# Optimization experiments

Measured on AMD Instinct MI355X. Metric: run time of the kernel, lower is better.

The kernel has to match this reference:

```python
import jax, jax.numpy as jnp
import numpy as np

N = 50000      # nodes
E = 800000     # edges
D_IN = 128     # raw feature dim
H = 96         # hidden_channels
K = 8          # experts
L = 4          # num_layers
C = 40         # classes


def setup_inputs() -> dict:
    key = jax.random.key(0)
    ks = jax.random.split(key, 10)
    stdv = 1.0 / np.sqrt(H)
    inp = {
        'x': jax.random.normal(ks[0], (N, D_IN), dtype=jnp.float32),
        'edge_index': jax.random.randint(ks[1], (2, E), 0, N, dtype=jnp.int64),
        # fcs[0]: Linear(d, hidden); fcs[1]: Linear(hidden, c)
        'fc0_w': jax.random.normal(ks[2], (D_IN, H), dtype=jnp.float32) * 0.05,
        'fc0_b': jnp.zeros((H,), dtype=jnp.float32),
        'fc1_w': jax.random.normal(ks[3], (H, C), dtype=jnp.float32) * 0.05,
        'fc1_b': jnp.zeros((C,), dtype=jnp.float32),
        # context_enc (method='node'): per-layer Linear(hidden, K)
        'ctx_w': jax.random.normal(ks[4], (L, H, K), dtype=jnp.float32) * 0.05,
        'ctx_b': jnp.zeros((L, K), dtype=jnp.float32),
        # GraphMultiConvolution weights: [L, K, hidden, hidden], uniform(-stdv, stdv)
        'conv_w': jax.random.uniform(ks[5], (L, K, H, H), dtype=jnp.float32,
                                     minval=-stdv, maxval=stdv),
    }
    return inp


def reference(x, edge_index, fc0_w, fc0_b, fc1_w, fc1_b, ctx_w, ctx_b, conv_w):
    # eval-mode forward (training=False): no dropout, softmax routing
    row = edge_index[0]
    col = edge_index[1]
    h = jax.nn.relu(x @ fc0_w + fc0_b)                     # [N, H]
    for i in range(L):
        # routing logits and soft expert weights z: [N, K]
        z = jax.nn.softmax(h @ ctx_w[i] + ctx_b[i], axis=-1)
        # spmm aggregation: hi[r] = sum over edges (r, c) of h[c]
        hi = jax.ops.segment_sum(h[col], row, num_segments=N)  # [N, H]
        # K-expert batched matmul: [N, K, H]
        outs = jnp.einsum('nd,kdo->nko', hi, conv_w[i])
        # gumbel/softmax-weighted combine + residual
        out = jnp.einsum('nk,nko->no', z, outs) + h
        h = jax.nn.relu(out)
    return h @ fc1_w + fc1_b                               # [N, C]
```

## Files before the change

### kernel.cpp

```cpp
#include <hip/hip_runtime.h>

#define N_NODES 50000
#define N_EDGES 800000
#define DIN     128
#define H       96
#define K_EXP   8
#define L_LAYERS 4
#define C_OUT   40

#define GSZ 6250

typedef _Float16 f16;
typedef f16 f16x2 __attribute__((ext_vector_type(2)));
typedef f16 f16x4 __attribute__((ext_vector_type(4)));
typedef f16 f16x8 __attribute__((ext_vector_type(8)));
typedef float f32x4 __attribute__((ext_vector_type(4)));


__global__ __launch_bounds__(256) void count_p(const int* __restrict__ row,
                                               int* __restrict__ deg,
                                               int* __restrict__ p, int e) {
    int i = blockIdx.x * blockDim.x + threadIdx.x;
    if (i < e) p[i] = atomicAdd(&deg[row[i]], 1);
}

__global__ __launch_bounds__(1024) void scanA(const int* __restrict__ deg,
                                              int* __restrict__ rowptr,
                                              int* __restrict__ partial, int n) {
    __shared__ int wsum[16];
    int tid  = threadIdx.x;
    int lane = tid & 63, wid = tid >> 6;
    int idx = blockIdx.x * 1024 + tid;
    int v = (idx < n) ? deg[idx] : 0;
    int s = v;
    #pragma unroll
    for (int off = 1; off < 64; off <<= 1) {
        int t = __shfl_up(s, off, 64);
        if (lane >= off) s += t;
    }
    if (lane == 63) wsum[wid] = s;
    __syncthreads();
    if (wid == 0 && lane < 16) {
        int w = wsum[lane];
        #pragma unroll
        for (int off = 1; off < 16; off <<= 1) {
            int t = __shfl_up(w, off, 16);
            if (lane >= off) w += t;
        }
        wsum[lane] = w;
    }
    __syncthreads();
    int waveoff = (wid == 0) ? 0 : wsum[wid - 1];
    if (idx < n) rowptr[idx + 1] = waveoff + s;
    if (tid == 1023) partial[blockIdx.x] = waveoff + s;
}

__global__ __launch_bounds__(1024) void scanC(int* __restrict__ rowptr,
                                              const int* __restrict__ partial,
                                              int nb, int n) {
    __shared__ int boff_s;
    int tid = threadIdx.x;
    if (tid < 64) {
        int v = (tid < nb && tid < (int)blockIdx.x) ? partial[tid] : 0;
        #pragma unroll
        for (int off = 32; off >= 1; off >>= 1) v += __shfl_xor(v, off, 64);
        if (tid == 0) boff_s = v;
    }
    __syncthreads();
    int boff = boff_s;
    int idx = blockIdx.x * 1024 + tid;
    if (idx == 0) rowptr[0] = 0;
    if (idx < n) rowptr[idx + 1] += boff;
}

__global__ __launch_bounds__(256) void scatter_store_xcd(const int* __restrict__ row,
                                                         const int* __restrict__ col,
                                                         const int* __restrict__ p,
                                                         const int* __restrict__ rowptr,
                                                         int* __restrict__ csr, int e) {
    int g = blockIdx.x & 7;
    int rlo = g * GSZ, rhi = rlo + GSZ;
    int stride = (gridDim.x >> 3) * 256;
    for (int i = (blockIdx.x >> 3) * 256 + threadIdx.x; i < e; i += stride) {
        int r = row[i];
        if (r >= rlo && r < rhi)
            csr[rowptr[r] + p[i]] = col[i];
    }
}


#define CONV_TOT (L_LAYERS * K_EXP * H * H)
#define FC0_TOT  (DIN * H)
#define FC1_TOT  (48 * H)

__global__ void convert_all(const float* __restrict__ conv_w,
                            const float* __restrict__ fc0_w,
                            const float* __restrict__ fc1_w,
                            f16* __restrict__ wfrag, f16* __restrict__ fc0t,
                            f16* __restrict__ fc1t) {
    int i = blockIdx.x * blockDim.x + threadIdx.x;
    if (i < CONV_TOT) {
        int o = i % H;
        int t = i / H;
        int d = t % H;
        int lk = t / H;
        int ct = o >> 4, lc = o & 15;
        int ks = d >> 5, quad = (d >> 3) & 3, j = d & 7;
        wfrag[(size_t)lk * 9216 + ct * 1536 + ks * 512 + (quad * 16 + lc) * 8 + j] =
            (f16)conv_w[i];
    } else if (i < CONV_TOT + FC0_TOT) {
        int j = i - CONV_TOT;
        int o = j % H, d = j / H;
        fc0t[o * DIN + d] = (f16)fc0_w[j];
    } else if (i < CONV_TOT + FC0_TOT + FC1_TOT) {
        int j = i - CONV_TOT - FC0_TOT;
        int o = j / H, d = j % H;
        fc1t[j] = (o < C_OUT) ? (f16)fc1_w[d * C_OUT + o] : (f16)0.f;
    }
}


#define SPMM_BLOCKS ((N_NODES + 31) / 32)
#define CTX_BLOCKS  ((N_NODES + 255) / 256)

__global__ __launch_bounds__(256) void layer_pre(const f16* __restrict__ h16,
                                                 const int* __restrict__ rowptr,
                                                 const int* __restrict__ csr,
                                                 f16* __restrict__ hi16,
                                                 const float* __restrict__ cw,
                                                 const float* __restrict__ cb,
                                                 float* __restrict__ zt, int n) {
    __shared__ float ws[H * K_EXP];
    __shared__ float bs[K_EXP];
    int tid = threadIdx.x;
    if ((int)blockIdx.x < SPMM_BLOCKS) {
        int r0 = blockIdx.x * 32 + (tid >> 4);
        int r1 = r0 + 16;
        int li = tid & 15;
        if (r0 >= n) return;
        int j0 = rowptr[r0], e0 = rowptr[r0 + 1];
        int j1 = 0, e1 = 0;
        if (r1 < n) { j1 = rowptr[r1]; e1 = rowptr[r1 + 1]; }
        bool act = li < 12;
        float accA[8] = {}, accB[8] = {};
        for (;;) {
            int m0 = e0 - j0; if (m0 > 16) m0 = 16;
            int m1 = e1 - j1; if (m1 > 16) m1 = 16;
            if (m0 <= 0 && m1 <= 0) break;
            int c0 = 0, c1 = 0;
            if (li < m0) c0 = csr[j0 + li];
            if (li < m1) c1 = csr[j1 + li];
            int mm = m0 > m1 ? m0 : m1;
            int t = 0;
            for (; t + 2 <= mm; t += 2) {
                int cc0a = __shfl(c0, t, 16),     cc1a = __shfl(c1, t, 16);
                int cc0b = __shfl(c0, t + 1, 16), cc1b = __shfl(c1, t + 1, 16);
                bool a0a = act && (t < m0),     a1a = act && (t < m1);
                bool a0b = act && (t + 1 < m0), a1b = act && (t + 1 < m1);
                f16x8 v0a = {}, v1a = {}, v0b = {}, v1b = {};
                if (a0a) v0a = *(const f16x8*)(h16 + (size_t)cc0a * H + li * 8);
                if (a1a) v1a = *(const f16x8*)(h16 + (size_t)cc1a * H + li * 8);
                if (a0b) v0b = *(const f16x8*)(h16 + (size_t)cc0b * H + li * 8);
                if (a1b) v1b = *(const f16x8*)(h16 + (size_t)cc1b * H + li * 8);
                if (a0a) {
                    #pragma unroll
                    for (int q = 0; q < 8; q++) accA[q] += (float)v0a[q];
                }
                if (a1a) {
                    #pragma unroll
                    for (int q = 0; q < 8; q++) accB[q] += (float)v1a[q];
                }
                if (a0b) {
                    #pragma unroll
                    for (int q = 0; q < 8; q++) accA[q] += (float)v0b[q];
                }
                if (a1b) {
                    #pragma unroll
                    for (int q = 0; q < 8; q++) accB[q] += (float)v1b[q];
                }
            }
            if (t < mm) {
                int cc0 = __shfl(c0, t, 16), cc1 = __shfl(c1, t, 16);
                bool a0 = act && (t < m0), a1 = act && (t < m1);
                f16x8 v0 = {}, v1 = {};
                if (a0) v0 = *(const f16x8*)(h16 + (size_t)cc0 * H + li * 8);
                if (a1) v1 = *(const f16x8*)(h16 + (size_t)cc1 * H + li * 8);
                if (a0) {
                    #pragma unroll
                    for (int q = 0; q < 8; q++) accA[q] += (float)v0[q];
                }
                if (a1) {
                    #pragma unroll
                    for (int q = 0; q < 8; q++) accB[q] += (float)v1[q];
                }
            }
            j0 += m0; j1 += m1;
        }
        if (act) {
            f16x8 oA;
            #pragma unroll
            for (int q = 0; q < 8; q++) oA[q] = (f16)accA[q];
            *(f16x8*)(hi16 + (size_t)r0 * H + li * 8) = oA;
            if (r1 < n) {
                f16x8 oB;
                #pragma unroll
                for (int q = 0; q < 8; q++) oB[q] = (f16)accB[q];
                *(f16x8*)(hi16 + (size_t)r1 * H + li * 8) = oB;
            }
        }
    } else {
        for (int t = tid; t < H * K_EXP; t += 256) ws[t] = cw[t];
        if (tid < K_EXP) bs[tid] = cb[tid];
        __syncthreads();
        int node = ((int)blockIdx.x - SPMM_BLOCKS) * 256 + tid;
        if (node >= n) return;
        float acc[K_EXP];
        #pragma unroll
        for (int k = 0; k < K_EXP; k++) acc[k] = bs[k];
        const f16* hr = h16 + (size_t)node * H;
        #pragma unroll 3
        for (int c8 = 0; c8 < 12; c8++) {
            f16x8 v = *(const f16x8*)(hr + c8 * 8);
            #pragma unroll
            for (int j = 0; j < 8; j++) {
                float hv = (float)v[j];
                int d = c8 * 8 + j;
                #pragma unroll
                for (int k = 0; k < K_EXP; k++) acc[k] += hv * ws[d * K_EXP + k];
            }
        }
        float mx = acc[0];
        #pragma unroll
        for (int k = 1; k < K_EXP; k++) mx = fmaxf(mx, acc[k]);
        float s = 0.f;
        #pragma unroll
        for (int k = 0; k < K_EXP; k++) { acc[k] = __expf(acc[k] - mx); s += acc[k]; }
        float inv = 1.f / s;
        #pragma unroll
        for (int k = 0; k < K_EXP; k++)
            zt[(size_t)k * N_NODES + node] = acc[k] * inv;
    }
}


#define FPAD 136

__global__ __launch_bounds__(256) void fc0_kernel(const float* __restrict__ x,
                                                  const f16* __restrict__ fc0t,
                                                  const float* __restrict__ b,
                                                  f16* __restrict__ h16, int n) {
    __shared__ f16 As[64 * FPAD];
    __shared__ f16 Ws[96 * FPAD];
    int tid = threadIdx.x;
    int l = tid & 63, w = tid >> 6;
    int quad = l >> 4, lc = l & 15;
    int row0 = blockIdx.x * 64;

    for (int t = tid; t < 2048; t += 256) {
        int m = t >> 5, c4 = (t & 31) * 4;
        int gr = row0 + m;
        float4 v = {0.f, 0.f, 0.f, 0.f};
        if (gr < n) v = *(const float4*)(x + (size_t)gr * DIN + c4);
        f16x4 h4 = {(f16)v.x, (f16)v.y, (f16)v.z, (f16)v.w};
        *(f16x4*)&As[m * FPAD + c4] = h4;
    }
    for (int t = tid; t < 1536; t += 256) {
        int o = t >> 4, c8 = (t & 15) * 8;
        *(f16x8*)&Ws[o * FPAD + c8] = *(const f16x8*)(fc0t + o * DIN + c8);
    }
    __syncthreads();

    f16x8 afr[4];
    #pragma unroll
    for (int ks = 0; ks < 4; ks++)
        afr[ks] = *(const f16x8*)&As[(16 * w + lc) * FPAD + ks * 32 + quad * 8];

    f32x4 acc[6] = {};
    #pragma unroll
    for (int ct = 0; ct < 6; ct++) {
        #pragma unroll
        for (int ks = 0; ks < 4; ks++) {
            f16x8 bfr = *(const f16x8*)&Ws[(ct * 16 + lc) * FPAD + ks * 32 + quad * 8];
            acc[ct] = __builtin_amdgcn_mfma_f32_16x16x32_f16(afr[ks], bfr, acc[ct], 0, 0, 0);
        }
    }

    int m0 = 16 * w + quad * 4;
    #pragma unroll
    for (int r = 0; r < 4; r++) {
        int gr = row0 + m0 + r;
        if (gr < n) {
            #pragma unroll
            for (int ct = 0; ct < 6; ct++) {
                int o = ct * 16 + lc;
                h16[(size_t)gr * H + o] = (f16)fmaxf(acc[ct][r] + b[o], 0.f);
            }
        }
    }
}


#define EG_STAGE 2
#define EG_HALFS (EG_STAGE * 9216)

__global__ __launch_bounds__(256) void expert_gemm(const f16* __restrict__ hi16,
                                                   const f16* __restrict__ hin16,
                                                   const f16* __restrict__ wfrag,
                                                   const float* __restrict__ zt,
                                                   f16* __restrict__ hout16, int n) {
    __shared__ f16 Wl[EG_HALFS];
    int tid = threadIdx.x;
    int l = tid & 63, w = tid >> 6;
    int quad = l >> 4, lc = l & 15;
    int wrow0 = blockIdx.x * 64 + w * 16;

    f16x8 afr[3];
    #pragma unroll
    for (int ks = 0; ks < 3; ks++)
        afr[ks] = *(const f16x8*)(hi16 + (size_t)(wrow0 + lc) * H + ks * 32 + quad * 8);

    f32x4 acc[6] = {};

    for (int kb = 0; kb < K_EXP; kb += EG_STAGE) {
        __syncthreads();
        const f16* src = wfrag + (size_t)kb * 9216;
        for (int t = tid; t < EG_HALFS / 8; t += 256)
            *(f16x8*)&Wl[t * 8] = *(const f16x8*)(src + t * 8);
        __syncthreads();

        #pragma unroll
        for (int k2 = 0; k2 < EG_STAGE; k2++) {
            int k = kb + k2;
            f32x4 zf = *(const f32x4*)(zt + (size_t)k * N_NODES + wrow0 + quad * 4);
            #pragma unroll
            for (int ct = 0; ct < 6; ct++) {
                f16x8 b0 = *(const f16x8*)&Wl[k2 * 9216 + ct * 1536 + 0 * 512 + l * 8];
                f16x8 b1 = *(const f16x8*)&Wl[k2 * 9216 + ct * 1536 + 1 * 512 + l * 8];
                f16x8 b2 = *(const f16x8*)&Wl[k2 * 9216 + ct * 1536 + 2 * 512 + l * 8];
                f32x4 tmp = {};
                tmp = __builtin_amdgcn_mfma_f32_16x16x32_f16(afr[0], b0, tmp, 0, 0, 0);
                tmp = __builtin_amdgcn_mfma_f32_16x16x32_f16(afr[1], b1, tmp, 0, 0, 0);
                tmp = __builtin_amdgcn_mfma_f32_16x16x32_f16(afr[2], b2, tmp, 0, 0, 0);
                acc[ct] += zf * tmp;
            }
        }
    }

    #pragma unroll
    for (int r = 0; r < 4; r++) {
        int gr = wrow0 + quad * 4 + r;
        if (gr < n) {
            #pragma unroll
            for (int ct = 0; ct < 6; ct++) {
                int o = ct * 16 + lc;
                float v = fmaxf(acc[ct][r] + (float)hin16[(size_t)gr * H + o], 0.f);
                hout16[(size_t)gr * H + o] = (f16)v;
            }
        }
    }
}


#define APAD 104

__global__ __launch_bounds__(256) void fc1_kernel(const f16* __restrict__ h16,
                                                  const f16* __restrict__ fc1t,
                                                  const float* __restrict__ b,
                                                  float* __restrict__ out, int n) {
    __shared__ f16 As[64 * APAD];
    __shared__ f16 Ws[48 * APAD];
    int tid = threadIdx.x;
    int l = tid & 63, w = tid >> 6;
    int quad = l >> 4, lc = l & 15;
    int row0 = blockIdx.x * 64;

    for (int t = tid; t < 768; t += 256) {
        int m = t / 12, c8 = (t % 12) * 8;
        int gr = row0 + m;
        f16x8 v = {};
        if (gr < n) v = *(const f16x8*)(h16 + (size_t)gr * H + c8);
        *(f16x8*)&As[m * APAD + c8] = v;
    }
    for (int t = tid; t < 576; t += 256) {
        int o = t / 12, c8 = (t % 12) * 8;
        *(f16x8*)&Ws[o * APAD + c8] = *(const f16x8*)(fc1t + o * H + c8);
    }
    __syncthreads();

    f16x8 afr[3];
    #pragma unroll
    for (int ks = 0; ks < 3; ks++)
        afr[ks] = *(const f16x8*)&As[(16 * w + lc) * APAD + ks * 32 + quad * 8];

    f32x4 acc[3] = {};
    #pragma unroll
    for (int ct = 0; ct < 3; ct++) {
        #pragma unroll
        for (int ks = 0; ks < 3; ks++) {
            f16x8 bfr = *(const f16x8*)&Ws[(ct * 16 + lc) * APAD + ks * 32 + quad * 8];
            acc[ct] = __builtin_amdgcn_mfma_f32_16x16x32_f16(afr[ks], bfr, acc[ct], 0, 0, 0);
        }
    }

    int m0 = 16 * w + quad * 4;
    #pragma unroll
    for (int r = 0; r < 4; r++) {
        int gr = row0 + m0 + r;
        if (gr < n) {
            #pragma unroll
            for (int ct = 0; ct < 3; ct++) {
                int o = ct * 16 + lc;
                if (o < C_OUT)
                    out[(size_t)gr * C_OUT + o] = acc[ct][r] + b[o];
            }
        }
    }
}


extern "C" void kernel_launch(void* const* d_in, const int* in_sizes, int n_in,
                              void* d_out, int out_size, void* d_ws, size_t ws_size,
                              hipStream_t stream) {
    const float* x      = (const float*)d_in[0];
    const int*   ei     = (const int*)d_in[1];
    const float* fc0_w  = (const float*)d_in[2];
    const float* fc0_b  = (const float*)d_in[3];
    const float* fc1_w  = (const float*)d_in[4];
    const float* fc1_b  = (const float*)d_in[5];
    const float* ctx_w  = (const float*)d_in[6];
    const float* ctx_b  = (const float*)d_in[7];
    const float* conv_w = (const float*)d_in[8];
    float* out = (float*)d_out;

    const size_t NH = (size_t)N_NODES * H;

    float* zbuf = (float*)d_ws;
    f16*   h16a = (f16*)(zbuf + (size_t)N_NODES * K_EXP);
    f16*   h16b = h16a + NH;
    f16*   hi16 = h16b + NH;
    f16*   wfrag= hi16 + NH;
    f16*   fc0t = wfrag + CONV_TOT;
    f16*   fc1t = fc0t + FC0_TOT;
    int* rowptr = (int*)(fc1t + FC1_TOT);
    int* deg    = rowptr + (N_NODES + 1);
    int* csr    = deg + N_NODES;
    int* prank  = csr + N_EDGES;
    int* partial  = prank + N_EDGES;

    const int* row = ei;
    const int* col = ei + N_EDGES;

    hipMemsetAsync(deg, 0, sizeof(int) * N_NODES, stream);

    count_p<<<(N_EDGES + 255) / 256, 256, 0, stream>>>(row, deg, prank, N_EDGES);
    int nsb = (N_NODES + 1023) / 1024;
    scanA<<<nsb, 1024, 0, stream>>>(deg, rowptr, partial, N_NODES);
    scanC<<<nsb, 1024, 0, stream>>>(rowptr, partial, nsb, N_NODES);
    scatter_store_xcd<<<1024, 256, 0, stream>>>(row, col, prank, rowptr, csr, N_EDGES);

    int ctotal = CONV_TOT + FC0_TOT + FC1_TOT;
    convert_all<<<(ctotal + 255) / 256, 256, 0, stream>>>(conv_w, fc0_w, fc1_w, wfrag, fc0t, fc1t);

    int gemm_grid = (N_NODES + 63) / 64;
    fc0_kernel<<<gemm_grid, 256, 0, stream>>>(x, fc0t, fc0_b, h16a, N_NODES);

    f16* hcur = h16a;
    f16* hnext = h16b;
    for (int i = 0; i < L_LAYERS; i++) {
        layer_pre<<<SPMM_BLOCKS + CTX_BLOCKS, 256, 0, stream>>>(
            hcur, rowptr, csr, hi16,
            ctx_w + (size_t)i * H * K_EXP, ctx_b + (size_t)i * K_EXP, zbuf, N_NODES);
        expert_gemm<<<gemm_grid, 256, 0, stream>>>(
            hi16, hcur, wfrag + (size_t)i * K_EXP * H * H, zbuf, hnext, N_NODES);
        f16* t = hcur; hcur = hnext; hnext = t;
    }
    fc1_kernel<<<gemm_grid, 256, 0, stream>>>(hcur, fc1t, fc1_b, out, N_NODES);
}
```

Measured before the change: 375.7 us.

## Bucket CSR neighbors by source-column range and sync blocks per bucket in SpMM

Builds the CSR with each row's edges split into 7 buckets keyed by the source column's high bits (8192-node ranges), so every row is stored as per-bucket segments. The SpMM walks the buckets in order and puts a block barrier after each one, so all warps in a block gather from the same slice of h at the same time, aiming for better cache locality. The cost is a scan over 8x more segment counters (400k entries with a larger partial-sum reduction), extra rowptr loads and barriers per row in SpMM, and more loop overhead for the short per-bucket edge lists.

```diff
diff --git a/kernel.cpp b/kernel.cpp
--- a/kernel.cpp
+++ b/kernel.cpp
@@ -10,6 +10,11 @@
 
 #define GSZ 6250
 
+#define NB_SHIFT 13
+#define NBUCK    7
+#define SEG_STRIDE 8
+#define NSEG (N_NODES * SEG_STRIDE)
+
 typedef _Float16 f16;
 typedef f16 f16x2 __attribute__((ext_vector_type(2)));
 typedef f16 f16x4 __attribute__((ext_vector_type(4)));
@@ -18,10 +23,14 @@
 
 
 __global__ __launch_bounds__(256) void count_p(const int* __restrict__ row,
+                                               const int* __restrict__ col,
                                                int* __restrict__ deg,
                                                int* __restrict__ p, int e) {
     int i = blockIdx.x * blockDim.x + threadIdx.x;
-    if (i < e) p[i] = atomicAdd(&deg[row[i]], 1);
+    if (i < e) {
+        int seg = row[i] * SEG_STRIDE + (col[i] >> NB_SHIFT);
+        p[i] = atomicAdd(&deg[seg], 1);
+    }
 }
 
 __global__ __launch_bounds__(1024) void scanA(const int* __restrict__ deg,
@@ -61,7 +70,8 @@
     __shared__ int boff_s;
     int tid = threadIdx.x;
     if (tid < 64) {
-        int v = (tid < nb && tid < (int)blockIdx.x) ? partial[tid] : 0;
+        int v = 0;
+        for (int j = tid; j < (int)blockIdx.x; j += 64) v += partial[j];
         #pragma unroll
         for (int off = 32; off >= 1; off >>= 1) v += __shfl_xor(v, off, 64);
         if (tid == 0) boff_s = v;
@@ -83,8 +93,11 @@
     int stride = (gridDim.x >> 3) * 256;
     for (int i = (blockIdx.x >> 3) * 256 + threadIdx.x; i < e; i += stride) {
         int r = row[i];
-        if (r >= rlo && r < rhi)
-            csr[rowptr[r] + p[i]] = col[i];
+        if (r >= rlo && r < rhi) {
+            int c = col[i];
+            int seg = r * SEG_STRIDE + (c >> NB_SHIFT);
+            csr[rowptr[seg] + p[i]] = c;
+        }
     }
 }
 
@@ -137,71 +150,75 @@
         int r0 = blockIdx.x * 32 + (tid >> 4);
         int r1 = r0 + 16;
         int li = tid & 15;
-        if (r0 >= n) return;
-        int j0 = rowptr[r0], e0 = rowptr[r0 + 1];
-        int j1 = 0, e1 = 0;
-        if (r1 < n) { j1 = rowptr[r1]; e1 = rowptr[r1 + 1]; }
+        bool v0 = r0 < n, v1 = r1 < n;
+        int base0 = r0 * SEG_STRIDE, base1 = r1 * SEG_STRIDE;
         bool act = li < 12;
         float accA[8] = {}, accB[8] = {};
-        for (;;) {
-            int m0 = e0 - j0; if (m0 > 16) m0 = 16;
-            int m1 = e1 - j1; if (m1 > 16) m1 = 16;
-            if (m0 <= 0 && m1 <= 0) break;
-            int c0 = 0, c1 = 0;
-            if (li < m0) c0 = csr[j0 + li];
-            if (li < m1) c1 = csr[j1 + li];
-            int mm = m0 > m1 ? m0 : m1;
-            int t = 0;
-            for (; t + 2 <= mm; t += 2) {
-                int cc0a = __shfl(c0, t, 16),     cc1a = __shfl(c1, t, 16);
-                int cc0b = __shfl(c0, t + 1, 16), cc1b = __shfl(c1, t + 1, 16);
-                bool a0a = act && (t < m0),     a1a = act && (t < m1);
-                bool a0b = act && (t + 1 < m0), a1b = act && (t + 1 < m1);
-                f16x8 v0a = {}, v1a = {}, v0b = {}, v1b = {};
-                if (a0a) v0a = *(const f16x8*)(h16 + (size_t)cc0a * H + li * 8);
-                if (a1a) v1a = *(const f16x8*)(h16 + (size_t)cc1a * H + li * 8);
-                if (a0b) v0b = *(const f16x8*)(h16 + (size_t)cc0b * H + li * 8);
-                if (a1b) v1b = *(const f16x8*)(h16 + (size_t)cc1b * H + li * 8);
-                if (a0a) {
-                    #pragma unroll
-                    for (int q = 0; q < 8; q++) accA[q] += (float)v0a[q];
+        for (int b = 0; b < NBUCK; b++) {
+            int j0 = 0, e0 = 0, j1 = 0, e1 = 0;
+            if (v0) { j0 = rowptr[base0 + b]; e0 = rowptr[base0 + b + 1]; }
+            if (v1) { j1 = rowptr[base1 + b]; e1 = rowptr[base1 + b + 1]; }
+            for (;;) {
+                int m0 = e0 - j0; if (m0 > 16) m0 = 16;
+                int m1 = e1 - j1; if (m1 > 16) m1 = 16;
+                if (m0 <= 0 && m1 <= 0) break;
+                int c0 = 0, c1 = 0;
+                if (li < m0) c0 = csr[j0 + li];
+                if (li < m1) c1 = csr[j1 + li];
+                int mm = m0 > m1 ? m0 : m1;
+                int t = 0;
+                for (; t + 2 <= mm; t += 2) {
+                    int cc0a = __shfl(c0, t, 16),     cc1a = __shfl(c1, t, 16);
+                    int cc0b = __shfl(c0, t + 1, 16), cc1b = __shfl(c1, t + 1, 16);
+                    bool a0a = act && (t < m0),     a1a = act && (t < m1);
+                    bool a0b = act && (t + 1 < m0), a1b = act && (t + 1 < m1);
+                    f16x8 v0a = {}, v1a = {}, v0b = {}, v1b = {};
+                    if (a0a) v0a = *(const f16x8*)(h16 + (size_t)cc0a * H + li * 8);
+                    if (a1a) v1a = *(const f16x8*)(h16 + (size_t)cc1a * H + li * 8);
+                    if (a0b) v0b = *(const f16x8*)(h16 + (size_t)cc0b * H + li * 8);
+                    if (a1b) v1b = *(const f16x8*)(h16 + (size_t)cc1b * H + li * 8);
+                    if (a0a) {
+                        #pragma unroll
+                        for (int q = 0; q < 8; q++) accA[q] += (float)v0a[q];
+                    }
+                    if (a1a) {
+                        #pragma unroll
+                        for (int q = 0; q < 8; q++) accB[q] += (float)v1a[q];
+                    }
+                    if (a0b) {
+                        #pragma unroll
+                        for (int q = 0; q < 8; q++) accA[q] += (float)v0b[q];
+                    }
+                    if (a1b) {
+                        #pragma unroll
+                        for (int q = 0; q < 8; q++) accB[q] += (float)v1b[q];
+                    }
                 }
-                if (a1a) {
-                    #pragma unroll
-                    for (int q = 0; q < 8; q++) accB[q] += (float)v1a[q];
+                if (t < mm) {
+                    int cc0 = __shfl(c0, t, 16), cc1 = __shfl(c1, t, 16);
+                    bool a0 = act && (t < m0), a1 = act && (t < m1);
+                    f16x8 va = {}, vb = {};
+                    if (a0) va = *(const f16x8*)(h16 + (size_t)cc0 * H + li * 8);
+                    if (a1) vb = *(const f16x8*)(h16 + (size_t)cc1 * H + li * 8);
+                    if (a0) {
+                        #pragma unroll
+                        for (int q = 0; q < 8; q++) accA[q] += (float)va[q];
+                    }
+                    if (a1) {
+                        #pragma unroll
+                        for (int q = 0; q < 8; q++) accB[q] += (float)vb[q];
+                    }
                 }
-                if (a0b) {
-                    #pragma unroll
-                    for (int q = 0; q < 8; q++) accA[q] += (float)v0b[q];
-                }
-                if (a1b) {
-                    #pragma unroll
-                    for (int q = 0; q < 8; q++) accB[q] += (float)v1b[q];
-                }
-            }
-            if (t < mm) {
-                int cc0 = __shfl(c0, t, 16), cc1 = __shfl(c1, t, 16);
-                bool a0 = act && (t < m0), a1 = act && (t < m1);
-                f16x8 v0 = {}, v1 = {};
-                if (a0) v0 = *(const f16x8*)(h16 + (size_t)cc0 * H + li * 8);
-                if (a1) v1 = *(const f16x8*)(h16 + (size_t)cc1 * H + li * 8);
-                if (a0) {
-                    #pragma unroll
-                    for (int q = 0; q < 8; q++) accA[q] += (float)v0[q];
-                }
-                if (a1) {
-                    #pragma unroll
-                    for (int q = 0; q < 8; q++) accB[q] += (float)v1[q];
-                }
-            }
-            j0 += m0; j1 += m1;
-        }
-        if (act) {
+                j0 += m0; j1 += m1;
+            }
+            __syncthreads();
+        }
+        if (act && v0) {
             f16x8 oA;
             #pragma unroll
             for (int q = 0; q < 8; q++) oA[q] = (f16)accA[q];
             *(f16x8*)(hi16 + (size_t)r0 * H + li * 8) = oA;
-            if (r1 < n) {
+            if (v1) {
                 f16x8 oB;
                 #pragma unroll
                 for (int q = 0; q < 8; q++) oB[q] = (f16)accB[q];
@@ -442,20 +459,20 @@
     f16*   fc0t = wfrag + CONV_TOT;
     f16*   fc1t = fc0t + FC0_TOT;
     int* rowptr = (int*)(fc1t + FC1_TOT);
-    int* deg    = rowptr + (N_NODES + 1);
-    int* csr    = deg + N_NODES;
+    int* deg    = rowptr + (NSEG + 1);
+    int* csr    = deg + NSEG;
     int* prank  = csr + N_EDGES;
     int* partial  = prank + N_EDGES;
 
     const int* row = ei;
     const int* col = ei + N_EDGES;
 
-    hipMemsetAsync(deg, 0, sizeof(int) * N_NODES, stream);
-
-    count_p<<<(N_EDGES + 255) / 256, 256, 0, stream>>>(row, deg, prank, N_EDGES);
-    int nsb = (N_NODES + 1023) / 1024;
-    scanA<<<nsb, 1024, 0, stream>>>(deg, rowptr, partial, N_NODES);
-    scanC<<<nsb, 1024, 0, stream>>>(rowptr, partial, nsb, N_NODES);
+    hipMemsetAsync(deg, 0, sizeof(int) * NSEG, stream);
+
+    count_p<<<(N_EDGES + 255) / 256, 256, 0, stream>>>(row, col, deg, prank, N_EDGES);
+    int nsb = (NSEG + 1023) / 1024;
+    scanA<<<nsb, 1024, 0, stream>>>(deg, rowptr, partial, NSEG);
+    scanC<<<nsb, 1024, 0, stream>>>(rowptr, partial, nsb, NSEG);
     scatter_store_xcd<<<1024, 256, 0, stream>>>(row, col, prank, rowptr, csr, N_EDGES);
 
     int ctotal = CONV_TOT + FC0_TOT + FC1_TOT;
```

New measurement: 445.0 us. 1.18x slower.

## Pad node feature rows to 128 halves and simplify SpMM to one row per group

Applied to the files above, without the earlier changes.

Node feature buffers (h and hi) now use a row stride of 128 halves instead of 96, so each row is 256-byte aligned and all 16 lanes can load unconditionally in the gather. The SpMM gather is rewritten to handle one destination row per 16-lane group with a 4-way unrolled edge loop, doubling the block count and removing the two-row interleave and its per-lane predicates. The scanC partial sum now loops over all preceding blocks rather than only the first 64. The padding raises the memory footprint and the bytes fetched per gathered row, and the padding lanes read columns that are never written.

```diff
diff --git a/kernel.cpp b/kernel.cpp
--- a/kernel.cpp
+++ b/kernel.cpp
@@ -4,6 +4,7 @@
 #define N_EDGES 800000
 #define DIN     128
 #define H       96
+#define HS      128
 #define K_EXP   8
 #define L_LAYERS 4
 #define C_OUT   40
@@ -61,7 +62,8 @@
     __shared__ int boff_s;
     int tid = threadIdx.x;
     if (tid < 64) {
-        int v = (tid < nb && tid < (int)blockIdx.x) ? partial[tid] : 0;
+        int v = 0;
+        for (int j = tid; j < (int)blockIdx.x; j += 64) v += partial[j];
         #pragma unroll
         for (int off = 32; off >= 1; off >>= 1) v += __shfl_xor(v, off, 64);
         if (tid == 0) boff_s = v;
@@ -120,7 +122,7 @@
 }
 
 
-#define SPMM_BLOCKS ((N_NODES + 31) / 32)
+#define SPMM_BLOCKS ((N_NODES + 15) / 16)
 #define CTX_BLOCKS  ((N_NODES + 255) / 256)
 
 __global__ __launch_bounds__(256) void layer_pre(const f16* __restrict__ h16,
@@ -134,79 +136,46 @@
     __shared__ float bs[K_EXP];
     int tid = threadIdx.x;
     if ((int)blockIdx.x < SPMM_BLOCKS) {
-        int r0 = blockIdx.x * 32 + (tid >> 4);
-        int r1 = r0 + 16;
+        int r  = blockIdx.x * 16 + (tid >> 4);
         int li = tid & 15;
-        if (r0 >= n) return;
-        int j0 = rowptr[r0], e0 = rowptr[r0 + 1];
-        int j1 = 0, e1 = 0;
-        if (r1 < n) { j1 = rowptr[r1]; e1 = rowptr[r1 + 1]; }
-        bool act = li < 12;
-        float accA[8] = {}, accB[8] = {};
-        for (;;) {
-            int m0 = e0 - j0; if (m0 > 16) m0 = 16;
-            int m1 = e1 - j1; if (m1 > 16) m1 = 16;
-            if (m0 <= 0 && m1 <= 0) break;
-            int c0 = 0, c1 = 0;
-            if (li < m0) c0 = csr[j0 + li];
-            if (li < m1) c1 = csr[j1 + li];
-            int mm = m0 > m1 ? m0 : m1;
+        if (r >= n) return;
+        int j = rowptr[r], e = rowptr[r + 1];
+        float acc[8] = {};
+        const f16* hb = h16 + li * 8;
+        while (j < e) {
+            int m = e - j; if (m > 16) m = 16;
+            int c = 0;
+            if (li < m) c = csr[j + li];
             int t = 0;
-            for (; t + 2 <= mm; t += 2) {
-                int cc0a = __shfl(c0, t, 16),     cc1a = __shfl(c1, t, 16);
-                int cc0b = __shfl(c0, t + 1, 16), cc1b = __shfl(c1, t + 1, 16);
-                bool a0a = act && (t < m0),     a1a = act && (t < m1);
-                bool a0b = act && (t + 1 < m0), a1b = act && (t + 1 < m1);
-                f16x8 v0a = {}, v1a = {}, v0b = {}, v1b = {};
-                if (a0a) v0a = *(const f16x8*)(h16 + (size_t)cc0a * H + li * 8);
-                if (a1a) v1a = *(const f16x8*)(h16 + (size_t)cc1a * H + li * 8);
-                if (a0b) v0b = *(const f16x8*)(h16 + (size_t)cc0b * H + li * 8);
-                if (a1b) v1b = *(const f16x8*)(h16 + (size_t)cc1b * H + li * 8);
-                if (a0a) {
-                    #pragma unroll
-                    for (int q = 0; q < 8; q++) accA[q] += (float)v0a[q];
-                }
-                if (a1a) {
-                    #pragma unroll
-                    for (int q = 0; q < 8; q++) accB[q] += (float)v1a[q];
-                }
-                if (a0b) {
-                    #pragma unroll
-                    for (int q = 0; q < 8; q++) accA[q] += (float)v0b[q];
-                }
-                if (a1b) {
-                    #pragma unroll
-                    for (int q = 0; q < 8; q++) accB[q] += (float)v1b[q];
-                }
-            }
-            if (t < mm) {
-                int cc0 = __shfl(c0, t, 16), cc1 = __shfl(c1, t, 16);
-                bool a0 = act && (t < m0), a1 = act && (t < m1);
-                f16x8 v0 = {}, v1 = {};
-                if (a0) v0 = *(const f16x8*)(h16 + (size_t)cc0 * H + li * 8);
-                if (a1) v1 = *(const f16x8*)(h16 + (size_t)cc1 * H + li * 8);
-                if (a0) {
-                    #pragma unroll
-                    for (int q = 0; q < 8; q++) accA[q] += (float)v0[q];
-                }
-                if (a1) {
-                    #pragma unroll
-                    for (int q = 0; q < 8; q++) accB[q] += (float)v1[q];
-                }
-            }
-            j0 += m0; j1 += m1;
-        }
-        if (act) {
-            f16x8 oA;
-            #pragma unroll
-            for (int q = 0; q < 8; q++) oA[q] = (f16)accA[q];
-            *(f16x8*)(hi16 + (size_t)r0 * H + li * 8) = oA;
-            if (r1 < n) {
-                f16x8 oB;
-                #pragma unroll
-                for (int q = 0; q < 8; q++) oB[q] = (f16)accB[q];
-                *(f16x8*)(hi16 + (size_t)r1 * H + li * 8) = oB;
-            }
+            for (; t + 4 <= m; t += 4) {
+                int c0 = __shfl(c, t, 16),     c1 = __shfl(c, t + 1, 16);
+                int c2 = __shfl(c, t + 2, 16), c3 = __shfl(c, t + 3, 16);
+                f16x8 v0 = *(const f16x8*)(hb + (size_t)c0 * HS);
+                f16x8 v1 = *(const f16x8*)(hb + (size_t)c1 * HS);
+                f16x8 v2 = *(const f16x8*)(hb + (size_t)c2 * HS);
+                f16x8 v3 = *(const f16x8*)(hb + (size_t)c3 * HS);
+                #pragma unroll
+                for (int q = 0; q < 8; q++) acc[q] += (float)v0[q];
+                #pragma unroll
+                for (int q = 0; q < 8; q++) acc[q] += (float)v1[q];
+                #pragma unroll
+                for (int q = 0; q < 8; q++) acc[q] += (float)v2[q];
+                #pragma unroll
+                for (int q = 0; q < 8; q++) acc[q] += (float)v3[q];
+            }
+            for (; t < m; t++) {
+                int cc = __shfl(c, t, 16);
+                f16x8 v = *(const f16x8*)(hb + (size_t)cc * HS);
+                #pragma unroll
+                for (int q = 0; q < 8; q++) acc[q] += (float)v[q];
+            }
+            j += m;
+        }
+        if (li < 12) {
+            f16x8 o;
+            #pragma unroll
+            for (int q = 0; q < 8; q++) o[q] = (f16)acc[q];
+            *(f16x8*)(hi16 + (size_t)r * HS + li * 8) = o;
         }
     } else {
         for (int t = tid; t < H * K_EXP; t += 256) ws[t] = cw[t];
@@ -217,7 +186,7 @@
         float acc[K_EXP];
         #pragma unroll
         for (int k = 0; k < K_EXP; k++) acc[k] = bs[k];
-        const f16* hr = h16 + (size_t)node * H;
+        const f16* hr = h16 + (size_t)node * HS;
         #pragma unroll 3
         for (int c8 = 0; c8 < 12; c8++) {
             f16x8 v = *(const f16x8*)(hr + c8 * 8);
@@ -293,7 +262,7 @@
             #pragma unroll
             for (int ct = 0; ct < 6; ct++) {
                 int o = ct * 16 + lc;
-                h16[(size_t)gr * H + o] = (f16)fmaxf(acc[ct][r] + b[o], 0.f);
+                h16[(size_t)gr * HS + o] = (f16)fmaxf(acc[ct][r] + b[o], 0.f);
             }
         }
     }
@@ -317,7 +286,7 @@
     f16x8 afr[3];
     #pragma unroll
     for (int ks = 0; ks < 3; ks++)
-        afr[ks] = *(const f16x8*)(hi16 + (size_t)(wrow0 + lc) * H + ks * 32 + quad * 8);
+        afr[ks] = *(const f16x8*)(hi16 + (size_t)(wrow0 + lc) * HS + ks * 32 + quad * 8);
 
     f32x4 acc[6] = {};
 
@@ -353,8 +322,8 @@
             #pragma unroll
             for (int ct = 0; ct < 6; ct++) {
                 int o = ct * 16 + lc;
-                float v = fmaxf(acc[ct][r] + (float)hin16[(size_t)gr * H + o], 0.f);
-                hout16[(size_t)gr * H + o] = (f16)v;
+                float v = fmaxf(acc[ct][r] + (float)hin16[(size_t)gr * HS + o], 0.f);
+                hout16[(size_t)gr * HS + o] = (f16)v;
             }
         }
     }
@@ -378,7 +347,7 @@
         int m = t / 12, c8 = (t % 12) * 8;
         int gr = row0 + m;
         f16x8 v = {};
-        if (gr < n) v = *(const f16x8*)(h16 + (size_t)gr * H + c8);
+        if (gr < n) v = *(const f16x8*)(h16 + (size_t)gr * HS + c8);
         *(f16x8*)&As[m * APAD + c8] = v;
     }
     for (int t = tid; t < 576; t += 256) {
@@ -432,7 +401,7 @@
     const float* conv_w = (const float*)d_in[8];
     float* out = (float*)d_out;
 
-    const size_t NH = (size_t)N_NODES * H;
+    const size_t NH = (size_t)N_NODES * HS;
 
     float* zbuf = (float*)d_ws;
     f16*   h16a = (f16*)(zbuf + (size_t)N_NODES * K_EXP);
```

After: 392.2 us. +4.4%, slower.
